# Kernel tuning notes

Measured on AMD Instinct MI355X. Metric: run time of the kernel, lower is better.

Reference implementation:

```python
import jax, jax.numpy as jnp
import numpy as np

B, T, E, H = 8, 2048, 512, 16
D = E // H  # 32 embeddings per head
LN_EPS = 1e-3  # keras LayerNormalization default epsilon
DECAY = 1.2


def setup_inputs() -> dict:
    key = jax.random.key(0)
    k0, k1, k2 = jax.random.split(key, 3)
    x = jax.random.normal(k0, (B, T, E), dtype=jnp.float32)
    W = jax.random.normal(k1, (E, E), dtype=jnp.float32) * (1.0 / np.sqrt(E))
    b = jnp.zeros((E,), dtype=jnp.float32)
    concept_map = jax.random.normal(k2, (H, D, D, D), dtype=jnp.float32) * 0.02
    gamma = jnp.ones((E,), dtype=jnp.float32)
    beta = jnp.zeros((E,), dtype=jnp.float32)
    return {"x": x, "W": W, "b": b, "concept_map": concept_map,
            "gamma": gamma, "beta": beta}


def reference(x, W, b, concept_map, gamma, beta):
    Bn, Tn, En = x.shape
    Hn = concept_map.shape[0]
    Dn = En // Hn
    # Dense projection, split into heads: (B,T,H,D)
    h = (jnp.einsum('bte,ef->btf', x, W) + b).reshape(Bn, Tn, Hn, Dn)
    # Decayed cumulative sum of preceding tokens: S_0 = 0, S_t = (S_{t-1} + h_{t-1}) / 1.2
    def step(s, h_t):
        return (s + h_t) / DECAY, s
    _, S = jax.lax.scan(step, jnp.zeros((Bn, Hn, Dn), h.dtype),
                        jnp.swapaxes(h, 0, 1))  # S: (T,B,H,D)
    S = jnp.swapaxes(S, 0, 1)  # (B,T,H,D)
    # Fused bilinear contraction: sum_{i,j} h[...,i] * S[...,j] * C[h,k,i,j]
    # (equivalent to outer-product * concept_map then reduce_sum over last two dims)
    y = jnp.einsum('bthi,bthj,hkij->bthk', h, S, concept_map) + h
    y = y.reshape(Bn, Tn, En)
    # LayerNormalization over last axis (keras default eps=1e-3)
    mu = jnp.mean(y, axis=-1, keepdims=True)
    var = jnp.var(y, axis=-1, keepdims=True)
    y = (y - mu) * jax.lax.rsqrt(var + LN_EPS) * gamma + beta
    # Dropout: identity at inference
    return y
```

## Files before the change

kernel.cpp:

```cpp
#include <hip/hip_runtime.h>
#include <hip/hip_bf16.h>

#define Bn 8
#define Tn 2048
#define En 512
#define Hn 16
#define Dn 32
#define NC 32
#define CL 64
#define NT (Bn*Tn)
#define INV_DECAY (1.0f/1.2f)

typedef __attribute__((ext_vector_type(8))) short  bf16x8;
typedef __attribute__((ext_vector_type(4))) float  f32x4;
typedef __attribute__((ext_vector_type(8))) unsigned short u16x8;

__device__ __forceinline__ unsigned short f2b(float f) {
    __hip_bfloat16 h = __float2bfloat16(f);
    return *reinterpret_cast<unsigned short*>(&h);
}
__device__ __forceinline__ float b2f(unsigned short u) {
    union { unsigned int i; float f; } c; c.i = ((unsigned int)u) << 16; return c.f;
}

__host__ __device__ constexpr float wpow(int e) {
    float r = 1.f;
    for (int i = 0; i < e; i++) r *= (1.0f / 1.2f);
    return r;
}

__device__ __forceinline__ size_t hm(int hd, int tok, int ch) {
    return (size_t)hd * ((size_t)NT * Dn) + (size_t)tok * Dn + ch;
}

__global__ __launch_bounds__(256) void prep_k(const float* __restrict__ C,
                                              unsigned short* __restrict__ Cl,
                                              const float* __restrict__ W,
                                              unsigned short* __restrict__ Wt) {
    __shared__ float tile[32][33];
    if (blockIdx.x < 256) {
        const int g = blockIdx.x * 256 + threadIdx.x;
        const int hd = g >> 12, rem = g & 4095;
        const int i = rem >> 7, half = (rem >> 6) & 1, lane = rem & 63;
        const int tloc = lane & 15, kgrp = lane >> 4;
        const int k = half * 16 + tloc;
        const float* src = C + (size_t)hd * 32768 + (size_t)k * 1024 + i * 32 + kgrp * 8;
        float4 a = reinterpret_cast<const float4*>(src)[0];
        float4 b = reinterpret_cast<const float4*>(src)[1];
        u16x8 st;
        st[0]=f2b(a.x); st[1]=f2b(a.y); st[2]=f2b(a.z); st[3]=f2b(a.w);
        st[4]=f2b(b.x); st[5]=f2b(b.y); st[6]=f2b(b.z); st[7]=f2b(b.w);
        *reinterpret_cast<u16x8*>(Cl + (size_t)g * 8) = st;
    } else {
        const int bid = blockIdx.x - 256;
        const int kb = (bid & 15) * 32, nb = (bid >> 4) * 32;
        const int tx = threadIdx.x & 31, ty = threadIdx.x >> 5;
        #pragma unroll
        for (int j = 0; j < 4; j++)
            tile[ty + 8 * j][tx] = W[(size_t)(kb + ty + 8 * j) * En + nb + tx];
        __syncthreads();
        #pragma unroll
        for (int j = 0; j < 4; j++)
            Wt[(size_t)(nb + ty + 8 * j) * En + kb + tx] = f2b(tile[tx][ty + 8 * j]);
    }
}

__global__ __launch_bounds__(256) void gemm_mfma_k(const float* __restrict__ x,
                                                   const unsigned short* __restrict__ Wt,
                                                   const float* __restrict__ bias,
                                                   unsigned short* __restrict__ h,
                                                   float* __restrict__ locals) {
    __shared__ unsigned short As[128][40];
    __shared__ unsigned short Bs[64][40];
    const int m0 = blockIdx.x * 128, n0 = blockIdx.y * 64;
    const int tid = threadIdx.x;
    const int wid = tid >> 6, lane = tid & 63;
    const int tloc = lane & 15, kgrp = lane >> 4;
    const int wr = wid >> 1, wc = wid & 1;

    const int ar = tid >> 1, ah = (tid & 1) * 16;
    const int brr = tid >> 2, bq = (tid & 3) * 8;

    f32x4 acc[4][2] = {};

    for (int k0 = 0; k0 < En; k0 += 32) {
        const float* xp = &x[(size_t)(m0 + ar) * En + k0 + ah];
        float4 a0 = reinterpret_cast<const float4*>(xp)[0];
        float4 a1 = reinterpret_cast<const float4*>(xp)[1];
        float4 a2 = reinterpret_cast<const float4*>(xp)[2];
        float4 a3 = reinterpret_cast<const float4*>(xp)[3];
        u16x8 bv = *reinterpret_cast<const u16x8*>(&Wt[(size_t)(n0 + brr) * En + k0 + bq]);
        __syncthreads();
        u16x8 w0, w1;
        w0[0]=f2b(a0.x); w0[1]=f2b(a0.y); w0[2]=f2b(a0.z); w0[3]=f2b(a0.w);
        w0[4]=f2b(a1.x); w0[5]=f2b(a1.y); w0[6]=f2b(a1.z); w0[7]=f2b(a1.w);
        w1[0]=f2b(a2.x); w1[1]=f2b(a2.y); w1[2]=f2b(a2.z); w1[3]=f2b(a2.w);
        w1[4]=f2b(a3.x); w1[5]=f2b(a3.y); w1[6]=f2b(a3.z); w1[7]=f2b(a3.w);
        *reinterpret_cast<u16x8*>(&As[ar][ah])     = w0;
        *reinterpret_cast<u16x8*>(&As[ar][ah + 8]) = w1;
        *reinterpret_cast<u16x8*>(&Bs[brr][bq])    = bv;
        __syncthreads();

        bf16x8 afr[4], bfr[2];
        #pragma unroll
        for (int m = 0; m < 4; m++)
            afr[m] = *reinterpret_cast<const bf16x8*>(&As[wr * 64 + m * 16 + tloc][kgrp * 8]);
        #pragma unroll
        for (int n = 0; n < 2; n++)
            bfr[n] = *reinterpret_cast<const bf16x8*>(&Bs[wc * 32 + n * 16 + tloc][kgrp * 8]);
        #pragma unroll
        for (int m = 0; m < 4; m++)
            #pragma unroll
            for (int n = 0; n < 2; n++)
                acc[m][n] = __builtin_amdgcn_mfma_f32_16x16x32_bf16(afr[m], bfr[n], acc[m][n], 0, 0, 0);
    }

    const float kmul = (kgrp & 1 ? 2.0736f : 1.f) * (kgrp & 2 ? 4.29981696f : 1.f);
    const int cg = blockIdx.x * 2 + wr;

    #pragma unroll
    for (int n = 0; n < 2; n++) {
        const int col = n0 + wc * 32 + n * 16 + tloc;
        const float bcol = bias[col];
        const int hd = col >> 5, ch = col & 31;
        float part = 0.f;
        #pragma unroll
        for (int m = 0; m < 4; m++)
            #pragma unroll
            for (int r = 0; r < 4; r++) {
                const int row = m0 + wr * 64 + m * 16 + kgrp * 4 + r;
                const unsigned short hb16 = f2b(acc[m][n][r] + bcol);
                h[hm(hd, row, ch)] = hb16;
                part += b2f(hb16) * (wpow(64 - m * 16 - r) * kmul);
            }
        part += __shfl_xor(part, 16);
        part += __shfl_xor(part, 32);
        if (kgrp == 0) locals[(size_t)cg * En + col] = part;
    }
}

__global__ __launch_bounds__(512) void scan_prefix_k(const float* __restrict__ locals,
                                                     float* __restrict__ Acar) {
    const int b = blockIdx.x;
    const int e = threadIdx.x;
    float invRL = 1.f;
    #pragma unroll
    for (int i = 0; i < CL; i++) invRL *= INV_DECAY;
    float A = 0.f;
    for (int c = 0; c < NC; c++) {
        Acar[(size_t)(b * NC + c) * En + e] = A;
        A = A * invRL + locals[(size_t)(b * NC + c) * En + e];
    }
}

__global__ __launch_bounds__(256, 3) void bilinear9_k(const unsigned short* __restrict__ hg,
                                                      const float* __restrict__ Acar,
                                                      unsigned short* __restrict__ yb,
                                                      const unsigned short* __restrict__ Cl) {
    __shared__ unsigned short hs[64][40];
    __shared__ unsigned short Ss[64][40];
    __shared__ float ys[4][64][36];

    const int hd = blockIdx.y;
    const int cg = blockIdx.x;
    const int tokens0 = cg * 64;
    const int tid = threadIdx.x;
    const int wid = tid >> 6, lane = tid & 63;
    const int tloc = lane & 15, kgrp = lane >> 4;
    const int j0 = kgrp * 8;

    bf16x8 afr[8][2];
    {
        const unsigned short* cb = Cl + (size_t)hd * 32768;
        #pragma unroll
        for (int s = 0; s < 8; s++) {
            const int i = wid * 8 + s;
            #pragma unroll
            for (int mt = 0; mt < 2; mt++)
                afr[s][mt] = *reinterpret_cast<const bf16x8*>(
                    cb + ((size_t)((i * 2 + mt) * 64 + lane) * 8));
        }
    }

    {
        const int tok = tid >> 2, c8 = (tid & 3) * 8;
        u16x8 v = *reinterpret_cast<const u16x8*>(hg + hm(hd, tokens0 + tok, c8));
        *reinterpret_cast<u16x8*>(&hs[tok][c8]) = v;
    }
    __syncthreads();

    if (tid < Dn) {
        float s = Acar[(size_t)cg * En + hd * Dn + tid];
        for (int t = 0; t < 64; t++) {
            Ss[t][tid] = f2b(s);
            s = (s + b2f(hs[t][tid])) * INV_DECAY;
        }
    }
    __syncthreads();

    u16x8 hreg[4];
    float sf[4][8];
    #pragma unroll
    for (int nt = 0; nt < 4; nt++) {
        const int trow = nt * 16 + tloc;
        hreg[nt] = *reinterpret_cast<const u16x8*>(&hs[trow][wid * 8]);
        u16x8 sv = *reinterpret_cast<const u16x8*>(&Ss[trow][j0]);
        #pragma unroll
        for (int e = 0; e < 8; e++) sf[nt][e] = b2f(sv[e]);
    }

    f32x4 acc[2][4] = {};
    #pragma unroll
    for (int s = 0; s < 8; s++) {
        #pragma unroll
        for (int nt = 0; nt < 4; nt++) {
            const float hsc = b2f(hreg[nt][s]);
            bf16x8 bfrag;
            #pragma unroll
            for (int e = 0; e < 8; e++) bfrag[e] = (short)f2b(hsc * sf[nt][e]);
            acc[0][nt] = __builtin_amdgcn_mfma_f32_16x16x32_bf16(afr[s][0], bfrag, acc[0][nt], 0, 0, 0);
            acc[1][nt] = __builtin_amdgcn_mfma_f32_16x16x32_bf16(afr[s][1], bfrag, acc[1][nt], 0, 0, 0);
        }
    }

    #pragma unroll
    for (int mt = 0; mt < 2; mt++)
        #pragma unroll
        for (int nt = 0; nt < 4; nt++)
            *reinterpret_cast<f32x4*>(&ys[wid][nt * 16 + tloc][mt * 16 + kgrp * 4]) = acc[mt][nt];
    __syncthreads();

    {
        const int token = tid >> 2, q = tid & 3;
        float y[8];
        #pragma unroll
        for (int e = 0; e < 8; e++) y[e] = 0.f;
        #pragma unroll
        for (int w = 0; w < 4; w++) {
            const float* src = &ys[w][token][q * 8];
            #pragma unroll
            for (int e = 0; e < 8; e++) y[e] += src[e];
        }
        u16x8 hres = *reinterpret_cast<const u16x8*>(&hs[token][q * 8]);
        u16x8 st;
        #pragma unroll
        for (int e = 0; e < 8; e++) st[e] = f2b(y[e] + b2f(hres[e]));
        *reinterpret_cast<u16x8*>(yb + hm(hd, tokens0 + token, q * 8)) = st;
    }
}

__global__ __launch_bounds__(256) void ln_k(const unsigned short* __restrict__ y,
                                            const float* __restrict__ gamma,
                                            const float* __restrict__ beta,
                                            float* __restrict__ out) {
    const int row = blockIdx.x * 4 + (threadIdx.x >> 6);
    const int lane = threadIdx.x & 63;
    u16x8 v = *reinterpret_cast<const u16x8*>(y + hm(lane >> 2, row, (lane & 3) * 8));
    float f[8];
    float s = 0.f, s2 = 0.f;
    #pragma unroll
    for (int e = 0; e < 8; e++) {
        f[e] = b2f(v[e]);
        s += f[e]; s2 += f[e] * f[e];
    }
    #pragma unroll
    for (int off = 1; off < 64; off <<= 1) {
        s  += __shfl_xor(s, off);
        s2 += __shfl_xor(s2, off);
    }
    const float mu = s * (1.f / En);
    const float var = s2 * (1.f / En) - mu * mu;
    const float rs = rsqrtf(var + 1e-3f);
    const int cbase = lane * 8;
    float4 g0 = reinterpret_cast<const float4*>(&gamma[cbase])[0];
    float4 g1 = reinterpret_cast<const float4*>(&gamma[cbase])[1];
    float4 b0 = reinterpret_cast<const float4*>(&beta[cbase])[0];
    float4 b1 = reinterpret_cast<const float4*>(&beta[cbase])[1];
    float4 o0, o1;
    o0.x = (f[0] - mu) * rs * g0.x + b0.x; o0.y = (f[1] - mu) * rs * g0.y + b0.y;
    o0.z = (f[2] - mu) * rs * g0.z + b0.z; o0.w = (f[3] - mu) * rs * g0.w + b0.w;
    o1.x = (f[4] - mu) * rs * g1.x + b1.x; o1.y = (f[5] - mu) * rs * g1.y + b1.y;
    o1.z = (f[6] - mu) * rs * g1.z + b1.z; o1.w = (f[7] - mu) * rs * g1.w + b1.w;
    float* op = out + (size_t)row * En;
    reinterpret_cast<float4*>(op)[lane * 2]     = o0;
    reinterpret_cast<float4*>(op)[lane * 2 + 1] = o1;
}

extern "C" void kernel_launch(void* const* d_in, const int* in_sizes, int n_in,
                              void* d_out, int out_size, void* d_ws, size_t ws_size,
                              hipStream_t stream) {
    const float* x     = (const float*)d_in[0];
    const float* W     = (const float*)d_in[1];
    const float* bias  = (const float*)d_in[2];
    const float* C     = (const float*)d_in[3];
    const float* gamma = (const float*)d_in[4];
    const float* beta  = (const float*)d_in[5];
    float* out = (float*)d_out;

    unsigned short* hb  = (unsigned short*)d_ws;
    unsigned short* yb  = hb + (size_t)Hn * NT * Dn;
    unsigned short* Cl  = yb + (size_t)Hn * NT * Dn;
    unsigned short* Wt  = Cl + (size_t)Hn * Dn * Dn * Dn;
    float* locals = (float*)(Wt + (size_t)En * En);
    float* Acar   = locals + (size_t)Bn * NC * En;

    prep_k<<<512, 256, 0, stream>>>(C, Cl, W, Wt);
    gemm_mfma_k<<<dim3(NT / 128, En / 64), 256, 0, stream>>>(x, Wt, bias, hb, locals);
    scan_prefix_k<<<Bn, 512, 0, stream>>>(locals, Acar);
    bilinear9_k<<<dim3(NT / CL, Hn), 256, 0, stream>>>(hb, Acar, yb, Cl);
    ln_k<<<NT / 4, 256, 0, stream>>>(yb, gamma, beta, out);
}
```

Baseline: 82.29 us.

## Parallelize intra-chunk decayed scan with wave shuffles and pad ys to stride 33

The serial 64-step per-channel scan, run by 32 threads inside the bilinear kernel, is replaced by a Hillis-Steele weighted prefix scan over all 256 threads using wavefront shuffles. The carry-in is applied through an exp2 decay factor. The ys staging buffer is padded to stride 33 with scalar stores to reduce LDS bank conflicts. The launch-bounds occupancy hint drops from 3 to 2. This targets the serial-scan bottleneck where most threads sat idle, at the cost of more shuffles and scalar LDS stores, plus small rounding differences from the reordered sums.

After: 81.80 us. About the same (-0.6%).

```diff
diff --git a/kernel.cpp b/kernel.cpp
--- a/kernel.cpp
+++ b/kernel.cpp
@@ -10,6 +10,7 @@
 #define CL 64
 #define NT (Bn*Tn)
 #define INV_DECAY (1.0f/1.2f)
+#define LOG2_INVD (-0.26303440583379383f)
 
 typedef __attribute__((ext_vector_type(8))) short  bf16x8;
 typedef __attribute__((ext_vector_type(4))) float  f32x4;
@@ -153,13 +154,13 @@
     }
 }
 
-__global__ __launch_bounds__(256, 3) void bilinear9_k(const unsigned short* __restrict__ hg,
-                                                      const float* __restrict__ Acar,
-                                                      unsigned short* __restrict__ yb,
-                                                      const unsigned short* __restrict__ Cl) {
+__global__ __launch_bounds__(256, 2) void bilinear10_k(const unsigned short* __restrict__ hg,
+                                                       const float* __restrict__ Acar,
+                                                       unsigned short* __restrict__ yb,
+                                                       const unsigned short* __restrict__ Cl) {
     __shared__ unsigned short hs[64][40];
     __shared__ unsigned short Ss[64][40];
-    __shared__ float ys[4][64][36];
+    __shared__ float ys[4][64][33];
 
     const int hd = blockIdx.y;
     const int cg = blockIdx.x;
@@ -168,6 +169,7 @@
     const int wid = tid >> 6, lane = tid & 63;
     const int tloc = lane & 15, kgrp = lane >> 4;
     const int j0 = kgrp * 8;
+    const int c0 = wid * 8;
 
     bf16x8 afr[8][2];
     {
@@ -182,19 +184,42 @@
         }
     }
 
+    float Ac[8];
+    #pragma unroll
+    for (int e = 0; e < 8; e++)
+        Ac[e] = Acar[(size_t)cg * En + hd * Dn + c0 + e];
+
     {
         const int tok = tid >> 2, c8 = (tid & 3) * 8;
-        u16x8 v = *reinterpret_cast<const u16x8*>(hg + hm(hd, tokens0 + tok, c8));
-        *reinterpret_cast<u16x8*>(&hs[tok][c8]) = v;
+        *reinterpret_cast<u16x8*>(&hs[tok][c8]) =
+            *reinterpret_cast<const u16x8*>(hg + hm(hd, tokens0 + tok, c8));
     }
     __syncthreads();
 
-    if (tid < Dn) {
-        float s = Acar[(size_t)cg * En + hd * Dn + tid];
-        for (int t = 0; t < 64; t++) {
-            Ss[t][tid] = f2b(s);
-            s = (s + b2f(hs[t][tid])) * INV_DECAY;
-        }
+    {
+        float P[8];
+        u16x8 hv = *reinterpret_cast<const u16x8*>(&hs[lane][c0]);
+        #pragma unroll
+        for (int e = 0; e < 8; e++) P[e] = b2f(hv[e]);
+        #pragma unroll
+        for (int k = 0; k < 6; k++) {
+            const int dlt = 1 << k;
+            const float wk = wpow(1 << k);
+            #pragma unroll
+            for (int e = 0; e < 8; e++) {
+                float o = __shfl_up(P[e], dlt, 64);
+                P[e] += (lane >= dlt) ? wk * o : 0.f;
+            }
+        }
+        const float dt = exp2f((float)lane * LOG2_INVD);
+        u16x8 sst;
+        #pragma unroll
+        for (int e = 0; e < 8; e++) {
+            float pm1 = __shfl_up(P[e], 1, 64);
+            if (lane == 0) pm1 = 0.f;
+            sst[e] = f2b(Ac[e] * dt + INV_DECAY * pm1);
+        }
+        *reinterpret_cast<u16x8*>(&Ss[lane][c0]) = sst;
     }
     __syncthreads();
 
@@ -203,7 +228,7 @@
     #pragma unroll
     for (int nt = 0; nt < 4; nt++) {
         const int trow = nt * 16 + tloc;
-        hreg[nt] = *reinterpret_cast<const u16x8*>(&hs[trow][wid * 8]);
+        hreg[nt] = *reinterpret_cast<const u16x8*>(&hs[trow][c0]);
         u16x8 sv = *reinterpret_cast<const u16x8*>(&Ss[trow][j0]);
         #pragma unroll
         for (int e = 0; e < 8; e++) sf[nt][e] = b2f(sv[e]);
@@ -227,7 +252,9 @@
     for (int mt = 0; mt < 2; mt++)
         #pragma unroll
         for (int nt = 0; nt < 4; nt++)
-            *reinterpret_cast<f32x4*>(&ys[wid][nt * 16 + tloc][mt * 16 + kgrp * 4]) = acc[mt][nt];
+            #pragma unroll
+            for (int r = 0; r < 4; r++)
+                ys[wid][nt * 16 + tloc][mt * 16 + kgrp * 4 + r] = acc[mt][nt][r];
     __syncthreads();
 
     {
@@ -237,9 +264,8 @@
         for (int e = 0; e < 8; e++) y[e] = 0.f;
         #pragma unroll
         for (int w = 0; w < 4; w++) {
-            const float* src = &ys[w][token][q * 8];
-            #pragma unroll
-            for (int e = 0; e < 8; e++) y[e] += src[e];
+            #pragma unroll
+            for (int e = 0; e < 8; e++) y[e] += ys[w][token][q * 8 + e];
         }
         u16x8 hres = *reinterpret_cast<const u16x8*>(&hs[token][q * 8]);
         u16x8 st;
@@ -307,6 +333,6 @@
     prep_k<<<512, 256, 0, stream>>>(C, Cl, W, Wt);
     gemm_mfma_k<<<dim3(NT / 128, En / 64), 256, 0, stream>>>(x, Wt, bias, hb, locals);
     scan_prefix_k<<<Bn, 512, 0, stream>>>(locals, Acar);
-    bilinear9_k<<<dim3(NT / CL, Hn), 256, 0, stream>>>(hb, Acar, yb, Cl);
+    bilinear10_k<<<dim3(NT / CL, Hn), 256, 0, stream>>>(hb, Acar, yb, Cl);
     ln_k<<<NT / 4, 256, 0, stream>>>(yb, gamma, beta, out);
 }
```
